# Optimization experiments

Measured on AMD Instinct MI355X. Metric: run time of the kernel, lower is better.

## Reference

```python
import jax, jax.numpy as jnp
import numpy as np

D_MODEL, D_K, D_V, N_HEADS = 1024, 64, 64, 16
BATCH, N_CTX = 2, 2048


def half_causal_allowed(n):
    # rows [0, n/2): attend to cols [0, n/2) only (dense block)
    # rows [n/2, n): standard causal (col <= row)
    i = jnp.arange(n)[:, None]
    j = jnp.arange(n)[None, :]
    top = (i < n // 2) & (j < n // 2)
    bot = (i >= n // 2) & (j <= i)
    return top | bot  # [n, n] bool


def setup_inputs() -> dict:
    key = jax.random.key(0)
    ks = jax.random.split(key, 8)
    s_in = 1.0 / np.sqrt(D_MODEL)
    s_out = 1.0 / np.sqrt(D_V * N_HEADS)
    return {
        "x": jax.random.normal(ks[0], (BATCH, N_CTX, D_MODEL), jnp.float32),
        # Linear weights stored [in, out] (transpose of torch layout)
        "Wq": jax.random.uniform(ks[1], (D_MODEL, D_K * N_HEADS), jnp.float32, -s_in, s_in),
        "bq": jax.random.uniform(ks[2], (D_K * N_HEADS,), jnp.float32, -s_in, s_in),
        "Wk": jax.random.uniform(ks[3], (D_MODEL, D_K * N_HEADS), jnp.float32, -s_in, s_in),
        "bk": jax.random.uniform(ks[4], (D_K * N_HEADS,), jnp.float32, -s_in, s_in),
        "Wv": jax.random.uniform(ks[5], (D_MODEL, D_V * N_HEADS), jnp.float32, -s_in, s_in),
        "bv": jax.random.uniform(ks[6], (D_V * N_HEADS,), jnp.float32, -s_in, s_in),
        "Wo": jax.random.uniform(ks[7], (D_V * N_HEADS, D_MODEL), jnp.float32, -s_out, s_out),
    }


def reference(x, Wq, bq, Wk, bk, Wv, bv, Wo):
    b, n, _ = x.shape
    h, dk, dv = N_HEADS, D_K, D_V
    # projections -> [b, h, n, d]
    q = (x @ Wq + bq).reshape(b, n, h, dk).transpose(0, 2, 1, 3)
    k = (x @ Wk + bk).reshape(b, n, h, dk).transpose(0, 2, 1, 3)
    v = (x @ Wv + bv).reshape(b, n, h, dv).transpose(0, 2, 1, 3)
    scores = jnp.einsum("bhqd,bhkd->bhqk", q / jnp.sqrt(jnp.float32(dk)), k)
    allowed = half_causal_allowed(n)  # [n, n]
    scores = jnp.where(allowed, scores, -jnp.inf)
    attn = jax.nn.softmax(scores, axis=-1)  # dropout p=0 -> identity
    out = jnp.einsum("bhqk,bhkd->bhqd", attn, v)
    out = out.transpose(0, 2, 1, 3).reshape(b, n, h * dv)
    return out @ Wo  # final Linear has no bias
```

## Files before the change

kernel.cpp:

```cpp
#include <hip/hip_runtime.h>
#include <hip/hip_bf16.h>

#define NH 16
#define DH 64
#define DM 1024
#define NC 2048
#define MROWS 4096
#define KVT 64

#define SCALE_Q 0.180336880f

typedef __attribute__((ext_vector_type(8))) short short8;
typedef __attribute__((ext_vector_type(4))) float f32x4;
typedef __attribute__((ext_vector_type(16))) float f32x16;
typedef __attribute__((ext_vector_type(4))) unsigned int uint4e;

__device__ __forceinline__ unsigned pkbf16(float a, float b) {
    unsigned r;
    asm("v_cvt_pk_bf16_f32 %0, %1, %2" : "=v"(r) : "v"(a), "v"(b));
    return r;
}
__device__ __forceinline__ unsigned short f2bf(float x) {
    return (unsigned short)(pkbf16(x, x) & 0xffffu);
}
__device__ __forceinline__ float exp2v(float x) {
    float r;
    asm("v_exp_f32 %0, %1" : "=v"(r) : "v"(x));
    return r;
}
__device__ __forceinline__ f32x16 fzero16() {
    f32x16 r;
    #pragma unroll
    for (int i = 0; i < 16; ++i) r[i] = 0.f;
    return r;
}
__device__ __forceinline__ short8 mk8(unsigned w0, unsigned w1, unsigned w2, unsigned w3) {
    uint4e u = {w0, w1, w2, w3};
    return __builtin_bit_cast(short8, u);
}
__device__ __forceinline__ void gload16(const unsigned short* g, unsigned short* l) {
    __builtin_amdgcn_global_load_lds(
        (const __attribute__((address_space(1))) void*)g,
        (__attribute__((address_space(3))) void*)l, 16, 0, 0);
}

__global__ __launch_bounds__(256) void prep(const float* __restrict__ x,
                                            const float* __restrict__ W0,
                                            const float* __restrict__ W1,
                                            const float* __restrict__ W2,
                                            const float* __restrict__ W3,
                                            unsigned short* __restrict__ xb,
                                            unsigned short* __restrict__ Wt4)
{
    __shared__ unsigned short T[64][72];
    const int bid = blockIdx.x;
    const int t = threadIdx.x;
    if (bid < 1024) {
        #pragma unroll
        for (int g = 0; g < 2; ++g) {
            const int i = bid * 512 + g * 256 + t;
            const float4 a = ((const float4*)x)[i * 2];
            const float4 b = ((const float4*)x)[i * 2 + 1];
            uint4e u = {pkbf16(a.x, a.y), pkbf16(a.z, a.w),
                        pkbf16(b.x, b.y), pkbf16(b.z, b.w)};
            ((uint4e*)xb)[i] = u;
        }
        return;
    }
    const int z = (bid - 1024) >> 8;
    const int tile = (bid - 1024) & 255;
    const int bi = tile >> 4, bj = tile & 15;
    const float* W = (z == 0) ? W0 : (z == 1) ? W1 : (z == 2) ? W2 : W3;
    unsigned short* Wt = Wt4 + (size_t)z * DM * DM;
    const int r = t >> 2, s = t & 3;
    const float* src = W + (size_t)(bi * 64 + r) * DM + bj * 64 + s * 16;
    float4 f0 = ((const float4*)src)[0];
    float4 f1 = ((const float4*)src)[1];
    float4 f2 = ((const float4*)src)[2];
    float4 f3 = ((const float4*)src)[3];
    uint2 u;
    u.x = pkbf16(f0.x, f0.y); u.y = pkbf16(f0.z, f0.w); *(uint2*)&T[r][s * 16]      = u;
    u.x = pkbf16(f1.x, f1.y); u.y = pkbf16(f1.z, f1.w); *(uint2*)&T[r][s * 16 + 4]  = u;
    u.x = pkbf16(f2.x, f2.y); u.y = pkbf16(f2.z, f2.w); *(uint2*)&T[r][s * 16 + 8]  = u;
    u.x = pkbf16(f3.x, f3.y); u.y = pkbf16(f3.z, f3.w); *(uint2*)&T[r][s * 16 + 12] = u;
    __syncthreads();
    unsigned short vals[16];
    #pragma unroll
    for (int j = 0; j < 16; ++j) vals[j] = T[s * 16 + j][r];
    unsigned short* dst = Wt + (size_t)(bj * 64 + r) * DM + bi * 64 + s * 16;
    *(short8*)(dst)     = *(short8*)&vals[0];
    *(short8*)(dst + 8) = *(short8*)&vals[8];
}

__global__ __launch_bounds__(256) void gemm_qkv(const unsigned short* __restrict__ A,
                                                const unsigned short* __restrict__ Bt,
                                                const float* __restrict__ bq,
                                                const float* __restrict__ bk,
                                                const float* __restrict__ bv,
                                                unsigned short* __restrict__ Out)
{
    __shared__ unsigned short As[128 * 32];
    __shared__ unsigned short Bs[128 * 32];
    const int t  = threadIdx.x;
    const int w  = t >> 6, l = t & 63;
    const int wr = w >> 1, wc = w & 1;
    const int m0 = blockIdx.y << 7;
    const int n0 = blockIdx.x << 7;

    f32x4 acc[4][4] = {};
    const int nkt = DM >> 5;
    for (int kt = 0; kt < nkt; ++kt) {
        #pragma unroll
        for (int j = 0; j < 2; ++j) {
            const int c0 = j * 256 + w * 64;
            const int cc = c0 + l;
            const int row = cc >> 2, qq = cc & 3;
            gload16(A  + (size_t)(m0 + row) * DM + kt * 32 + qq * 8, &As[c0 * 8]);
            gload16(Bt + (size_t)(n0 + row) * DM + kt * 32 + qq * 8, &Bs[c0 * 8]);
        }
        __syncthreads();
        short8 af[4], bf_[4];
        #pragma unroll
        for (int mi = 0; mi < 4; ++mi)
            af[mi] = *(short8*)&As[(wr * 64 + mi * 16 + (l & 15)) * 32 + (l >> 4) * 8];
        #pragma unroll
        for (int ni = 0; ni < 4; ++ni)
            bf_[ni] = *(short8*)&Bs[(wc * 64 + ni * 16 + (l & 15)) * 32 + (l >> 4) * 8];
        #pragma unroll
        for (int mi = 0; mi < 4; ++mi)
            #pragma unroll
            for (int ni = 0; ni < 4; ++ni)
                acc[mi][ni] = __builtin_amdgcn_mfma_f32_16x16x32_bf16(
                                  af[mi], bf_[ni], acc[mi][ni], 0, 0, 0);
        __syncthreads();
    }

    const int seg = n0 >> 10;
    const float* bias = (seg == 0) ? bq : (seg == 1) ? bk : bv;
    const float scale = (seg == 0) ? SCALE_Q : 1.0f;
    const int ncol0 = (n0 & 1023) + wc * 64;
    float bvv[4];
    #pragma unroll
    for (int ni = 0; ni < 4; ++ni)
        bvv[ni] = bias[ncol0 + ni * 16 + (l & 15)];

    if (seg == 2) {
        unsigned short* vt = Out + 2 * (size_t)MROWS * DM;
        #pragma unroll
        for (int mi = 0; mi < 4; ++mi)
            #pragma unroll
            for (int ni = 0; ni < 4; ++ni) {
                const int gcol = ncol0 + ni * 16 + (l & 15);
                const int h_ = gcol >> 6, d_ = gcol & 63;
                #pragma unroll
                for (int r = 0; r < 4; ++r) {
                    const int grow = m0 + wr * 64 + mi * 16 + (l >> 4) * 4 + r;
                    const int b_ = grow >> 11, n_ = grow & 2047;
                    vt[(((size_t)b_ * 16 + h_) * 64 + d_) * NC + n_] =
                        f2bf(acc[mi][ni][r] + bvv[ni]);
                }
            }
    } else {
        unsigned short* C = Out + (size_t)seg * MROWS * DM;
        #pragma unroll
        for (int mi = 0; mi < 4; ++mi)
            #pragma unroll
            for (int ni = 0; ni < 4; ++ni) {
                const int gcol = ncol0 + ni * 16 + (l & 15);
                #pragma unroll
                for (int r = 0; r < 4; ++r) {
                    const int grow = m0 + wr * 64 + mi * 16 + (l >> 4) * 4 + r;
                    C[(size_t)grow * DM + gcol] = f2bf((acc[mi][ni][r] + bvv[ni]) * scale);
                }
            }
    }
}

__global__ __launch_bounds__(256) void gemm_wo(const unsigned short* __restrict__ A,
                                               const unsigned short* __restrict__ Bt,
                                               float* __restrict__ C)
{
    __shared__ unsigned short As[64 * 32];
    __shared__ unsigned short Bs[128 * 32];
    const int t = threadIdx.x, w = t >> 6, l = t & 63;
    const int wr = w >> 1, wc = w & 1;
    const int m0 = blockIdx.y << 6;
    const int n0 = blockIdx.x << 7;

    f32x4 acc[2][4] = {};
    const int nkt = DM >> 5;
    for (int kt = 0; kt < nkt; ++kt) {
        {
            const int c0 = w * 64;
            const int cc = c0 + l;
            const int row = cc >> 2, qq = cc & 3;
            gload16(A + (size_t)(m0 + row) * DM + kt * 32 + qq * 8, &As[c0 * 8]);
        }
        #pragma unroll
        for (int j = 0; j < 2; ++j) {
            const int c0 = j * 256 + w * 64;
            const int cc = c0 + l;
            const int row = cc >> 2, qq = cc & 3;
            gload16(Bt + (size_t)(n0 + row) * DM + kt * 32 + qq * 8, &Bs[c0 * 8]);
        }
        __syncthreads();
        short8 af[2], bf_[4];
        #pragma unroll
        for (int mi = 0; mi < 2; ++mi)
            af[mi] = *(short8*)&As[(wr * 32 + mi * 16 + (l & 15)) * 32 + (l >> 4) * 8];
        #pragma unroll
        for (int ni = 0; ni < 4; ++ni)
            bf_[ni] = *(short8*)&Bs[(wc * 64 + ni * 16 + (l & 15)) * 32 + (l >> 4) * 8];
        #pragma unroll
        for (int mi = 0; mi < 2; ++mi)
            #pragma unroll
            for (int ni = 0; ni < 4; ++ni)
                acc[mi][ni] = __builtin_amdgcn_mfma_f32_16x16x32_bf16(
                                  af[mi], bf_[ni], acc[mi][ni], 0, 0, 0);
        __syncthreads();
    }
    #pragma unroll
    for (int mi = 0; mi < 2; ++mi)
        #pragma unroll
        for (int ni = 0; ni < 4; ++ni) {
            const int gcol = n0 + wc * 64 + ni * 16 + (l & 15);
            #pragma unroll
            for (int r = 0; r < 4; ++r) {
                const int grow = m0 + wr * 32 + mi * 16 + (l >> 4) * 4 + r;
                C[(size_t)grow * DM + gcol] = acc[mi][ni][r];
            }
        }
}

__global__ __launch_bounds__(128) void attn_split(const unsigned short* __restrict__ Qg,
                                                  const unsigned short* __restrict__ Kg,
                                                  const unsigned short* __restrict__ Vtg,
                                                  unsigned short* __restrict__ Og)
{
    __shared__ unsigned short KS[2][4096];
    __shared__ unsigned short VS[2][4096];
    const int t   = threadIdx.x;
    const int w   = t >> 6;
    const int l   = t & 63;
    const int l31 = l & 31;
    const int hi  = l >> 5;

    const int f   = blockIdx.x;
    const int xcd = f & 7;
    const int pos = f >> 3;
    const int bh  = xcd * 4 + (pos >> 6);
    int qc = pos & 63;
    if ((pos >> 6) & 1) qc = 63 - qc;
    const int b = bh >> 4;
    const int h = bh & 15;

    const int qb = qc << 5;
    const size_t rb0 = (size_t)b * NC;
    const int hd = h * DH;

    const unsigned short* qp = Qg + (rb0 + qb + l31) * DM + hd + hi * 8;
    short8 fq[4];
    #pragma unroll
    for (int c = 0; c < 4; ++c)
        fq[c] = *(const short8*)(qp + c * 16);

    f32x16 o0 = fzero16(), o1 = fzero16();
    f32x16 lacc = fzero16();
    const int nkv = (qc < 32) ? 16 : ((qc >> 1) + 1);
    const int niter = (nkv - w + 1) >> 1;

    const unsigned short* Vbase = Vtg + (size_t)bh * 64 * NC;

    auto stage = [&](int it) {
        const int kb = it * KVT;
        #pragma unroll
        for (int j = 0; j < 8; ++j) {
            const int p    = j * 64 + l;
            const int row  = p >> 3;
            const int slot = (p & 7) ^ (row & 7);
            gload16(Kg + (size_t)(rb0 + kb + row) * DM + hd + slot * 8,
                    &KS[w][j * 512]);
            gload16(Vbase + (size_t)row * NC + kb + slot * 8,
                    &VS[w][j * 512]);
        }
    };

    stage(w);

    for (int i = 0; i < niter; ++i) {
        const int it = w + 2 * i;
        const int kb = it * KVT;
        asm volatile("s_waitcnt vmcnt(0)" ::: "memory");

        short8 kf[2][4], vf[2][4];
        #pragma unroll
        for (int half = 0; half < 2; ++half) {
            const int row = half * 32 + l31;
            const int rx  = row & 7;
            #pragma unroll
            for (int c = 0; c < 4; ++c) {
                const int slot = (c * 2 + hi) ^ rx;
                kf[half][c] = *(const short8*)(&KS[w][row * 64 + slot * 8]);
                vf[half][c] = *(const short8*)(&VS[w][row * 64 + slot * 8]);
            }
        }
        asm volatile("s_waitcnt lgkmcnt(0)" ::: "memory");
        __builtin_amdgcn_sched_barrier(0);
        if (i + 1 < niter) stage(w + 2 * (i + 1));

        f32x16 s0 = fzero16(), s1 = fzero16();
        __builtin_amdgcn_s_setprio(1);
        #pragma unroll
        for (int c = 0; c < 4; ++c) {
            s0 = __builtin_amdgcn_mfma_f32_32x32x16_bf16(kf[0][c], fq[c], s0, 0, 0, 0);
            s1 = __builtin_amdgcn_mfma_f32_32x32x16_bf16(kf[1][c], fq[c], s1, 0, 0, 0);
        }
        __builtin_amdgcn_s_setprio(0);
        if (qc >= 32 && it == nkv - 1) {
            const int qg = qb + l31;
            #pragma unroll
            for (int r = 0; r < 16; ++r) {
                const int kk = (r & 3) + 8 * (r >> 2) + 4 * hi;
                if (kb + kk > qg)      s0[r] = -1e30f;
                if (kb + 32 + kk > qg) s1[r] = -1e30f;
            }
        }
        #pragma unroll
        for (int r = 0; r < 16; ++r) s0[r] = exp2v(s0[r]);
        #pragma unroll
        for (int r = 0; r < 16; ++r) s1[r] = exp2v(s1[r]);
        #pragma unroll
        for (int r = 0; r < 16; ++r) lacc[r] += s0[r] + s1[r];
        __builtin_amdgcn_s_setprio(1);
        #pragma unroll
        for (int kc = 0; kc < 4; ++kc) {
            const f32x16 src = (kc < 2) ? s0 : s1;
            const int rbase = (kc & 1) * 8;
            unsigned A01 = pkbf16(src[rbase + 0], src[rbase + 1]);
            unsigned A23 = pkbf16(src[rbase + 2], src[rbase + 3]);
            unsigned A45 = pkbf16(src[rbase + 4], src[rbase + 5]);
            unsigned A67 = pkbf16(src[rbase + 6], src[rbase + 7]);
            unsigned s01 = (unsigned)__shfl_xor((int)A01, 32);
            unsigned s23 = (unsigned)__shfl_xor((int)A23, 32);
            unsigned s45 = (unsigned)__shfl_xor((int)A45, 32);
            unsigned s67 = (unsigned)__shfl_xor((int)A67, 32);
            short8 fp = hi ? mk8(s45, s67, A45, A67)
                           : mk8(A01, A23, s01, s23);
            o0 = __builtin_amdgcn_mfma_f32_32x32x16_bf16(vf[0][kc], fp, o0, 0, 0, 0);
            o1 = __builtin_amdgcn_mfma_f32_32x32x16_bf16(vf[1][kc], fp, o1, 0, 0, 0);
        }
        __builtin_amdgcn_s_setprio(0);
    }

    float lr[8];
    #pragma unroll
    for (int r = 0; r < 8; ++r) lr[r] = lacc[r] + lacc[r + 8];
    #pragma unroll
    for (int st = 4; st > 0; st >>= 1)
        #pragma unroll
        for (int r = 0; r < 4; ++r)
            if (r < st) lr[r] += lr[r + st];
    const float lpart = lr[0] + __shfl_xor(lr[0], 32);

    {
        float* po = (float*)&KS[w][0];
        #pragma unroll
        for (int r = 0; r < 16; ++r) {
            po[l * 32 + r]      = o0[r];
            po[l * 32 + 16 + r] = o1[r];
        }
        ((float*)&VS[w][0])[l] = lpart;
    }
    __syncthreads();

    if (w == 0) {
        const float* po1 = (const float*)&KS[1][0];
        float oc0[16], oc1[16];
        #pragma unroll
        for (int r = 0; r < 16; ++r) {
            oc0[r] = o0[r] + po1[l * 32 + r];
            oc1[r] = o1[r] + po1[l * 32 + 16 + r];
        }
        const float lt = lpart + ((const float*)&VS[1][0])[l];
        const float inv = 1.f / lt;
        unsigned short* obuf = &VS[0][0];
        unsigned short* reg = obuf + (size_t)l31 * 72;
        #pragma unroll
        for (int r = 0; r < 16; ++r) {
            const int dd = (r & 3) + 8 * (r >> 2) + 4 * hi;
            reg[dd]      = f2bf(oc0[r] * inv);
            reg[dd + 32] = f2bf(oc1[r] * inv);
        }
        const int row = l >> 1, seg = l & 1;
        const unsigned short* src = obuf + (size_t)row * 72 + seg * 32;
        unsigned short* dst = Og + (rb0 + qb + row) * DM + hd + seg * 32;
        #pragma unroll
        for (int i = 0; i < 4; ++i)
            *(short8*)(dst + i * 8) = *(const short8*)(src + i * 8);
    }
}

extern "C" void kernel_launch(void* const* d_in, const int* in_sizes, int n_in,
                              void* d_out, int out_size, void* d_ws, size_t ws_size,
                              hipStream_t stream)
{
    const float* x  = (const float*)d_in[0];
    const float* Wq = (const float*)d_in[1];
    const float* bq = (const float*)d_in[2];
    const float* Wk = (const float*)d_in[3];
    const float* bk = (const float*)d_in[4];
    const float* Wv = (const float*)d_in[5];
    const float* bv = (const float*)d_in[6];
    const float* Wo = (const float*)d_in[7];
    float* out = (float*)d_out;

    char* ws = (char*)d_ws;
    const size_t szA = (size_t)MROWS * DM * 2;
    const size_t szW = (size_t)DM * DM * 2;
    unsigned short* xb  = (unsigned short*)(ws);
    unsigned short* wqT = (unsigned short*)(ws + szA);
    unsigned short* woT = (unsigned short*)(ws + szA + 3 * szW);
    unsigned short* qb_ = (unsigned short*)(ws + szA + 4 * szW);
    unsigned short* kb_ = (unsigned short*)(ws + 2 * szA + 4 * szW);
    unsigned short* vt_ = (unsigned short*)(ws + 3 * szA + 4 * szW);
    unsigned short* ab_ = (unsigned short*)(ws + 4 * szA + 4 * szW);

    prep<<<dim3(2048), 256, 0, stream>>>(x, Wq, Wk, Wv, Wo, xb, wqT);
    gemm_qkv<<<dim3(24, 32), 256, 0, stream>>>(xb, wqT, bq, bk, bv, qb_);
    attn_split<<<dim3(2048), 128, 0, stream>>>(qb_, kb_, vt_, ab_);
    gemm_wo<<<dim3(8, 64), 256, 0, stream>>>(ab_, woT, out);
}
```

Before: 118.9 us.

## Replace split-KV two-wave attention with single-wave 64-query tiles and double-buffered KV

New measurement: 132.8 us. 11.7% more time.

```diff
diff --git a/kernel.cpp b/kernel.cpp
--- a/kernel.cpp
+++ b/kernel.cpp
@@ -232,46 +232,48 @@
         }
 }
 
-__global__ __launch_bounds__(128) void attn_split(const unsigned short* __restrict__ Qg,
-                                                  const unsigned short* __restrict__ Kg,
-                                                  const unsigned short* __restrict__ Vtg,
-                                                  unsigned short* __restrict__ Og)
+__global__ __launch_bounds__(64) void attn_d64(const unsigned short* __restrict__ Qg,
+                                               const unsigned short* __restrict__ Kg,
+                                               const unsigned short* __restrict__ Vtg,
+                                               unsigned short* __restrict__ Og)
 {
     __shared__ unsigned short KS[2][4096];
     __shared__ unsigned short VS[2][4096];
-    const int t   = threadIdx.x;
-    const int w   = t >> 6;
-    const int l   = t & 63;
+    const int l   = threadIdx.x;
     const int l31 = l & 31;
     const int hi  = l >> 5;
 
     const int f   = blockIdx.x;
     const int xcd = f & 7;
     const int pos = f >> 3;
-    const int bh  = xcd * 4 + (pos >> 6);
-    int qc = pos & 63;
-    if ((pos >> 6) & 1) qc = 63 - qc;
+    const int bh  = xcd * 4 + (pos >> 5);
+    int qt = pos & 31;
+    if ((pos >> 5) & 1) qt = 31 - qt;
     const int b = bh >> 4;
     const int h = bh & 15;
 
-    const int qb = qc << 5;
+    const int qb = qt << 6;
     const size_t rb0 = (size_t)b * NC;
     const int hd = h * DH;
 
-    const unsigned short* qp = Qg + (rb0 + qb + l31) * DM + hd + hi * 8;
-    short8 fq[4];
-    #pragma unroll
-    for (int c = 0; c < 4; ++c)
-        fq[c] = *(const short8*)(qp + c * 16);
-
-    f32x16 o0 = fzero16(), o1 = fzero16();
-    f32x16 lacc = fzero16();
-    const int nkv = (qc < 32) ? 16 : ((qc >> 1) + 1);
-    const int niter = (nkv - w + 1) >> 1;
+    const unsigned short* qp0 = Qg + (rb0 + qb + l31) * DM + hd + hi * 8;
+    const unsigned short* qp1 = qp0 + (size_t)32 * DM;
+    short8 fq0[4], fq1[4];
+    #pragma unroll
+    for (int c = 0; c < 4; ++c) {
+        fq0[c] = *(const short8*)(qp0 + c * 16);
+        fq1[c] = *(const short8*)(qp1 + c * 16);
+    }
+
+    f32x16 o00 = fzero16(), o01 = fzero16();
+    f32x16 o10 = fzero16(), o11 = fzero16();
+    f32x16 lacc0 = fzero16(), lacc1 = fzero16();
+    const bool bottom = (qt >= 16);
+    const int nkv = bottom ? (qt + 1) : 16;
 
     const unsigned short* Vbase = Vtg + (size_t)bh * 64 * NC;
 
-    auto stage = [&](int it) {
+    auto stage = [&](int it, int buf) {
         const int kb = it * KVT;
         #pragma unroll
         for (int j = 0; j < 8; ++j) {
@@ -279,35 +281,15 @@
             const int row  = p >> 3;
             const int slot = (p & 7) ^ (row & 7);
             gload16(Kg + (size_t)(rb0 + kb + row) * DM + hd + slot * 8,
-                    &KS[w][j * 512]);
+                    &KS[buf][j * 512]);
             gload16(Vbase + (size_t)row * NC + kb + slot * 8,
-                    &VS[w][j * 512]);
+                    &VS[buf][j * 512]);
         }
     };
 
-    stage(w);
-
-    for (int i = 0; i < niter; ++i) {
-        const int it = w + 2 * i;
-        const int kb = it * KVT;
-        asm volatile("s_waitcnt vmcnt(0)" ::: "memory");
-
-        short8 kf[2][4], vf[2][4];
-        #pragma unroll
-        for (int half = 0; half < 2; ++half) {
-            const int row = half * 32 + l31;
-            const int rx  = row & 7;
-            #pragma unroll
-            for (int c = 0; c < 4; ++c) {
-                const int slot = (c * 2 + hi) ^ rx;
-                kf[half][c] = *(const short8*)(&KS[w][row * 64 + slot * 8]);
-                vf[half][c] = *(const short8*)(&VS[w][row * 64 + slot * 8]);
-            }
-        }
-        asm volatile("s_waitcnt lgkmcnt(0)" ::: "memory");
-        __builtin_amdgcn_sched_barrier(0);
-        if (i + 1 < niter) stage(w + 2 * (i + 1));
-
+    auto tile_compute = [&](const short8 kf[2][4], const short8 vf[2][4],
+                            const short8* fq, f32x16& oA, f32x16& oB,
+                            f32x16& lac, bool domask, int qrel) {
         f32x16 s0 = fzero16(), s1 = fzero16();
         __builtin_amdgcn_s_setprio(1);
         #pragma unroll
@@ -316,13 +298,12 @@
             s1 = __builtin_amdgcn_mfma_f32_32x32x16_bf16(kf[1][c], fq[c], s1, 0, 0, 0);
         }
         __builtin_amdgcn_s_setprio(0);
-        if (qc >= 32 && it == nkv - 1) {
-            const int qg = qb + l31;
+        if (domask) {
             #pragma unroll
             for (int r = 0; r < 16; ++r) {
                 const int kk = (r & 3) + 8 * (r >> 2) + 4 * hi;
-                if (kb + kk > qg)      s0[r] = -1e30f;
-                if (kb + 32 + kk > qg) s1[r] = -1e30f;
+                if (kk > qrel)      s0[r] = -1e30f;
+                if (32 + kk > qrel) s1[r] = -1e30f;
             }
         }
         #pragma unroll
@@ -330,7 +311,7 @@
         #pragma unroll
         for (int r = 0; r < 16; ++r) s1[r] = exp2v(s1[r]);
         #pragma unroll
-        for (int r = 0; r < 16; ++r) lacc[r] += s0[r] + s1[r];
+        for (int r = 0; r < 16; ++r) lac[r] += s0[r] + s1[r];
         __builtin_amdgcn_s_setprio(1);
         #pragma unroll
         for (int kc = 0; kc < 4; ++kc) {
@@ -346,57 +327,77 @@
             unsigned s67 = (unsigned)__shfl_xor((int)A67, 32);
             short8 fp = hi ? mk8(s45, s67, A45, A67)
                            : mk8(A01, A23, s01, s23);
-            o0 = __builtin_amdgcn_mfma_f32_32x32x16_bf16(vf[0][kc], fp, o0, 0, 0, 0);
-            o1 = __builtin_amdgcn_mfma_f32_32x32x16_bf16(vf[1][kc], fp, o1, 0, 0, 0);
+            oA = __builtin_amdgcn_mfma_f32_32x32x16_bf16(vf[0][kc], fp, oA, 0, 0, 0);
+            oB = __builtin_amdgcn_mfma_f32_32x32x16_bf16(vf[1][kc], fp, oB, 0, 0, 0);
         }
         __builtin_amdgcn_s_setprio(0);
-    }
-
-    float lr[8];
-    #pragma unroll
-    for (int r = 0; r < 8; ++r) lr[r] = lacc[r] + lacc[r + 8];
-    #pragma unroll
-    for (int st = 4; st > 0; st >>= 1)
-        #pragma unroll
-        for (int r = 0; r < 4; ++r)
-            if (r < st) lr[r] += lr[r + st];
-    const float lpart = lr[0] + __shfl_xor(lr[0], 32);
-
-    {
-        float* po = (float*)&KS[w][0];
-        #pragma unroll
-        for (int r = 0; r < 16; ++r) {
-            po[l * 32 + r]      = o0[r];
-            po[l * 32 + 16 + r] = o1[r];
-        }
-        ((float*)&VS[w][0])[l] = lpart;
-    }
-    __syncthreads();
-
-    if (w == 0) {
-        const float* po1 = (const float*)&KS[1][0];
-        float oc0[16], oc1[16];
-        #pragma unroll
-        for (int r = 0; r < 16; ++r) {
-            oc0[r] = o0[r] + po1[l * 32 + r];
-            oc1[r] = o1[r] + po1[l * 32 + 16 + r];
-        }
-        const float lt = lpart + ((const float*)&VS[1][0])[l];
+    };
+
+    stage(0, 0);
+    stage(1, 1);
+
+    for (int it = 0; it < nkv; ++it) {
+        const int cur = it & 1;
+        if (it + 1 < nkv) {
+            asm volatile("s_waitcnt vmcnt(16)" ::: "memory");
+        } else {
+            asm volatile("s_waitcnt vmcnt(0)" ::: "memory");
+        }
+
+        short8 kf[2][4], vf[2][4];
+        #pragma unroll
+        for (int half = 0; half < 2; ++half) {
+            const int row = half * 32 + l31;
+            const int rx  = row & 7;
+            #pragma unroll
+            for (int c = 0; c < 4; ++c) {
+                const int slot = (c * 2 + hi) ^ rx;
+                kf[half][c] = *(const short8*)(&KS[cur][row * 64 + slot * 8]);
+                vf[half][c] = *(const short8*)(&VS[cur][row * 64 + slot * 8]);
+            }
+        }
+        asm volatile("s_waitcnt lgkmcnt(0)" ::: "memory");
+        __builtin_amdgcn_sched_barrier(0);
+        if (it + 2 < nkv) stage(it + 2, cur);
+
+        const bool domask = bottom && (it == nkv - 1);
+        tile_compute(kf, vf, fq0, o00, o01, lacc0, domask, l31);
+        tile_compute(kf, vf, fq1, o10, o11, lacc1, domask, 32 + l31);
+    }
+
+    unsigned short* obuf = (unsigned short*)&KS[0][0];
+    #pragma unroll
+    for (int s = 0; s < 2; ++s) {
+        const f32x16& la = s ? lacc1 : lacc0;
+        const f32x16& oA = s ? o10 : o00;
+        const f32x16& oB = s ? o11 : o01;
+        float lr[8];
+        #pragma unroll
+        for (int r = 0; r < 8; ++r) lr[r] = la[r] + la[r + 8];
+        #pragma unroll
+        for (int st = 4; st > 0; st >>= 1)
+            #pragma unroll
+            for (int r = 0; r < 4; ++r)
+                if (r < st) lr[r] += lr[r + st];
+        const float lt = lr[0] + __shfl_xor(lr[0], 32);
         const float inv = 1.f / lt;
-        unsigned short* obuf = &VS[0][0];
-        unsigned short* reg = obuf + (size_t)l31 * 72;
-        #pragma unroll
-        for (int r = 0; r < 16; ++r) {
-            const int dd = (r & 3) + 8 * (r >> 2) + 4 * hi;
-            reg[dd]      = f2bf(oc0[r] * inv);
-            reg[dd + 32] = f2bf(oc1[r] * inv);
-        }
-        const int row = l >> 1, seg = l & 1;
-        const unsigned short* src = obuf + (size_t)row * 72 + seg * 32;
-        unsigned short* dst = Og + (rb0 + qb + row) * DM + hd + seg * 32;
-        #pragma unroll
-        for (int i = 0; i < 4; ++i)
-            *(short8*)(dst + i * 8) = *(const short8*)(src + i * 8);
+        {
+            unsigned short* reg = obuf + (size_t)l31 * 72;
+            #pragma unroll
+            for (int r = 0; r < 16; ++r) {
+                const int dd = (r & 3) + 8 * (r >> 2) + 4 * hi;
+                reg[dd]      = f2bf(oA[r] * inv);
+                reg[dd + 32] = f2bf(oB[r] * inv);
+            }
+        }
+        {
+            const int row = l >> 1, seg = l & 1;
+            const unsigned short* src = obuf + (size_t)row * 72 + seg * 32;
+            unsigned short* dst = Og + (rb0 + qb + s * 32 + row) * DM + hd + seg * 32;
+            #pragma unroll
+            for (int i = 0; i < 4; ++i)
+                *(short8*)(dst + i * 8) = *(const short8*)(src + i * 8);
+        }
     }
 }
 
@@ -427,6 +428,6 @@
 
     prep<<<dim3(2048), 256, 0, stream>>>(x, Wq, Wk, Wv, Wo, xb, wqT);
     gemm_qkv<<<dim3(24, 32), 256, 0, stream>>>(xb, wqT, bq, bk, bv, qb_);
-    attn_split<<<dim3(2048), 128, 0, stream>>>(qb_, kb_, vt_, ab_);
+    attn_d64<<<dim3(1024), 64, 0, stream>>>(qb_, kb_, vt_, ab_);
     gemm_wo<<<dim3(8, 64), 256, 0, stream>>>(ab_, woT, out);
 }
```
